# Kernel tuning notes

Hardware: AMD Instinct MI355X
Metric: run time of the kernel (lower is better)

Reference implementation:

```python
import jax, jax.numpy as jnp
import numpy as np

N = 50000
E = 800000
IN_DIM = 64          # 'in_dim'; ndata h has dim 2*in_dim, p has dim in_dim
EDGE_DIM = 32
OUT_DIM = 64
AVG_D_LOG = 2.8332   # avg_d['log'] = log(avg_degree + 1), avg_degree = 16
EPS_STD = 1e-5
EPS_BN = 1e-5


def setup_inputs() -> dict:
    key = jax.random.key(0)
    ks = jax.random.split(key, 16)
    def glorot(k, fan_in, fan_out):
        lim = np.sqrt(6.0 / (fan_in + fan_out)).astype(np.float32)
        return jax.random.uniform(k, (fan_in, fan_out), jnp.float32, -lim, lim)
    d_pre_h = 2 * 2 * IN_DIM + EDGE_DIM   # 288
    d_pre_p = 2 * IN_DIM + EDGE_DIM       # 160
    d_post_h = (4 * 3 + 2) * IN_DIM       # 896
    d_post_p = (4 * 3 + 1) * IN_DIM       # 832
    return {
        "h": jax.random.normal(ks[0], (N, 2 * IN_DIM), jnp.float32),
        "p": jax.random.normal(ks[1], (N, IN_DIM), jnp.float32),
        "e": jax.random.normal(ks[2], (E, EDGE_DIM), jnp.float32),
        "src": jax.random.randint(ks[3], (E,), 0, N, jnp.int32),
        "dst": jax.random.randint(ks[4], (E,), 0, N, jnp.int32),
        "snorm_n": jax.random.uniform(ks[5], (N, 1), jnp.float32, 0.05, 1.0),
        "W_pre_h": glorot(ks[6], d_pre_h, IN_DIM),
        "b_pre_h": jnp.zeros((IN_DIM,), jnp.float32),
        "W_pre_p": glorot(ks[7], d_pre_p, IN_DIM),
        "b_pre_p": jnp.zeros((IN_DIM,), jnp.float32),
        "W_post_h": glorot(ks[8], d_post_h, OUT_DIM),
        "b_post_h": jnp.zeros((OUT_DIM,), jnp.float32),
        "W_post_p": glorot(ks[9], d_post_p, OUT_DIM),
        "b_post_p": jnp.zeros((OUT_DIM,), jnp.float32),
        "bn_gamma": jnp.ones((OUT_DIM,), jnp.float32),
        "bn_beta": jnp.zeros((OUT_DIM,), jnp.float32),
    }


def _agg_scale(msg, dst, deg):
    # msg: [E, d] edge messages reduced at dst; PNA aggregators mean/max/min/std
    degc = jnp.maximum(deg, 1.0)
    s = jax.ops.segment_sum(msg, dst, num_segments=N)
    mean = s / degc[:, None]
    sq = jax.ops.segment_sum(msg * msg, dst, num_segments=N) / degc[:, None]
    var = jax.nn.relu(sq - mean * mean)
    std = jnp.sqrt(var + EPS_STD)
    has = (deg > 0)[:, None]
    mx = jnp.where(has, jax.ops.segment_max(msg, dst, num_segments=N), 0.0)
    mn = jnp.where(has, jax.ops.segment_min(msg, dst, num_segments=N), 0.0)
    agg = jnp.concatenate([mean, mx, mn, std], axis=1)  # [N, 4d]
    logd = jnp.where(deg > 0, jnp.log(deg + 1.0), 1.0)
    amp = (logd / AVG_D_LOG)[:, None]
    att = (AVG_D_LOG / logd)[:, None]
    # scalers: identity, amplification, attenuation -> [N, 12d]
    return jnp.concatenate([agg, agg * amp, agg * att], axis=1)


def reference(h, p, e, src, dst, snorm_n,
              W_pre_h, b_pre_h, W_pre_p, b_pre_p,
              W_post_h, b_post_h, W_post_p, b_post_p,
              bn_gamma, bn_beta):
    # pretrans (1-layer MLP == linear) on concatenated edge endpoint features
    z_h = jnp.concatenate([h[src], h[dst], e], axis=1)   # [E, 4*in+edge]
    z_p = jnp.concatenate([p[src], p[dst], e], axis=1)   # [E, 2*in+edge]
    e_for_h = z_h @ W_pre_h + b_pre_h                    # [E, in]
    e_for_p = z_p @ W_pre_p + b_pre_p                    # [E, in]

    deg = jax.ops.segment_sum(jnp.ones((E,), jnp.float32), dst, num_segments=N)
    agg_h = _agg_scale(e_for_h, dst, deg)                # [N, 12*in]
    agg_p = _agg_scale(e_for_p, dst, deg)                # [N, 12*in]

    h_cat = jnp.concatenate([h, agg_h], axis=1)          # [N, 14*in]
    p_cat = jnp.concatenate([p, agg_p], axis=1)          # [N, 13*in]
    h_out = h_cat @ W_post_h + b_post_h                  # [N, out]
    p_out = p_cat @ W_post_p + b_post_p                  # [N, out]

    # graph norm
    h_out = h_out * snorm_n
    # batch norm (training-mode batch statistics, biased variance)
    mu = jnp.mean(h_out, axis=0)
    var = jnp.mean((h_out - mu) ** 2, axis=0)
    h_out = (h_out - mu) / jnp.sqrt(var + EPS_BN) * bn_gamma + bn_beta
    # dropout = identity (eval / p=0)
    return h_out, p_out
```

## Files before the change

kernel.cpp:

```cpp
#include <hip/hip_runtime.h>
#include <hip/hip_bf16.h>
#include <hip/hip_fp16.h>


#define N_NODES 50000
#define N_EDGES 800000
#define NS 3200000
#define AVG_D_LOG 2.8332f

typedef unsigned short u16;
typedef unsigned int u32;
typedef __attribute__((ext_vector_type(8))) short short8;
typedef __attribute__((ext_vector_type(4))) float f32x4;

__device__ __forceinline__ float bflo(u32 u) { return __uint_as_float(u << 16); }
__device__ __forceinline__ float bfhi(u32 u) { return __uint_as_float(u & 0xffff0000u); }
__device__ __forceinline__ float bf2f(u16 u) { return __uint_as_float(((u32)u) << 16); }
__device__ __forceinline__ u16 f2bf(float x) {
  u32 u = __float_as_uint(x);
  return (u16)((u + 0x7fff + ((u >> 16) & 1)) >> 16);
}
__device__ __forceinline__ float hlo(u32 u) { return __half2float(__ushort_as_half((u16)(u & 0xffffu))); }
__device__ __forceinline__ float hhi(u32 u) { return __half2float(__ushort_as_half((u16)(u >> 16))); }

__device__ __forceinline__ int is_bf(const void* gamma) {
  return ((const u32*)gamma)[0] == 0x3F803F80u ? 1 : 0;
}

__device__ __forceinline__ f32x4 mfma16(short8 a, short8 b, f32x4 c) {
  return __builtin_amdgcn_mfma_f32_16x16x32_bf16(a, b, c, 0, 0, 0);
}

__device__ __forceinline__ void load8(float z[8], const void* base, size_t off,
                                      int bf) {
  if (bf) {
    uint4 u = *(const uint4*)((const u16*)base + off);
    z[0] = bflo(u.x); z[1] = bfhi(u.x); z[2] = bflo(u.y); z[3] = bfhi(u.y);
    z[4] = bflo(u.z); z[5] = bfhi(u.z); z[6] = bflo(u.w); z[7] = bfhi(u.w);
  } else {
    const float* f = (const float*)base + off;
    float4 a = *(const float4*)f;
    float4 b = *(const float4*)(f + 4);
    z[0] = a.x; z[1] = a.y; z[2] = a.z; z[3] = a.w;
    z[4] = b.x; z[5] = b.y; z[6] = b.z; z[7] = b.w;
  }
}

__device__ __forceinline__ float load1(const void* base, size_t off, int bf) {
  return bf ? bf2f(((const u16*)base)[off]) : ((const float*)base)[off];
}

__device__ __forceinline__ short8 cvt8bf(const float z[8]) {
  union { __hip_bfloat162 b[4]; short8 s; } u;
  u.b[0] = __float22bfloat162_rn(make_float2(z[0], z[1]));
  u.b[1] = __float22bfloat162_rn(make_float2(z[2], z[3]));
  u.b[2] = __float22bfloat162_rn(make_float2(z[4], z[5]));
  u.b[3] = __float22bfloat162_rn(make_float2(z[6], z[7]));
  return u.s;
}

__device__ __forceinline__ u32 packh2(float a, float b) {
  union { __half2 h; u32 u; } x;
  x.h = __float22half2_rn(make_float2(a, b));
  return x.u;
}

__device__ __forceinline__ int sem(int o) {
  return ((o >> 4) & 3) * 64 + (o >> 6) * 16 + (o & 15);
}

__global__ __launch_bounds__(256) void k_convert(
    const void* __restrict__ Wpreh, const void* __restrict__ Wprep,
    const void* __restrict__ Wposth, const void* __restrict__ Wpostp,
    const void* __restrict__ bpreh, const void* __restrict__ bprep,
    const void* __restrict__ bposth, const void* __restrict__ bpostp,
    const void* __restrict__ gamma, float* __restrict__ bias,
    u16* __restrict__ frag) {
  int i = blockIdx.x * 256 + threadIdx.x;
  if (i >= 256 + 139264) return;
  int bf = is_bf(gamma);
  if (i < 256) {
    const void* s = (i < 64) ? bpreh : (i < 128) ? bprep : (i < 192) ? bposth : bpostp;
    bias[i] = load1(s, i & 63, bf);
    return;
  }
  int g = i - 256;
  const void* W; int fidx, rowoff, post = 0;
  if (g < 8192)        { W = Wpreh;  fidx = g;          rowoff = 0; }
  else if (g < 16384)  { W = Wpreh;  fidx = g - 8192;   rowoff = 128; }
  else if (g < 20480)  { W = Wprep;  fidx = g - 16384;  rowoff = 0; }
  else if (g < 24576)  { W = Wprep;  fidx = g - 20480;  rowoff = 64; }
  else if (g < 81920)  { W = Wposth; fidx = g - 24576;  rowoff = 0; post = 1; }
  else if (g < 135168) { W = Wpostp; fidx = g - 81920;  rowoff = 0; post = 2; }
  else if (g < 137216) { W = Wpreh;  fidx = g - 135168; rowoff = 256; }
  else                 { W = Wprep;  fidx = g - 137216; rowoff = 128; }
  int f = fidx;
  int kc = f >> 11, nt = (f >> 9) & 3, lane = (f >> 3) & 63, j = f & 7;
  int k = kc * 32 + (lane >> 4) * 8 + j;
  int n = nt * 16 + (lane & 15);
  int row;
  if (post == 1) {
    row = (k < 128) ? k
        : (k < 384) ? 128 + sem(k - 128)
        : (k < 640) ? 384 + sem(k - 384)
                    : 640 + sem(k - 640);
  } else if (post == 2) {
    row = (k < 64) ? k
        : (k < 320) ? 64 + sem(k - 64)
        : (k < 576) ? 320 + sem(k - 320)
                    : 576 + sem(k - 576);
  } else {
    row = rowoff + k;
  }
  frag[g] = f2bf(load1(W, (size_t)row * 64 + n, bf));
}

__global__ __launch_bounds__(256) void k_hist(const int* __restrict__ dst,
                                              int* __restrict__ cnt) {
  int i = blockIdx.x * 256 + threadIdx.x;
  if (i < N_EDGES) atomicAdd(cnt + dst[i], 1);
}

__global__ __launch_bounds__(1024) void k_scan1(const int* __restrict__ cnt,
                                                int* __restrict__ offs,
                                                int* __restrict__ bsum) {
  __shared__ int buf[1024];
  int t = threadIdx.x;
  int i = blockIdx.x * 1024 + t;
  int v = (i < N_NODES) ? cnt[i] : 0;
  buf[t] = v;
  __syncthreads();
#pragma unroll
  for (int d = 1; d < 1024; d <<= 1) {
    int x = (t >= d) ? buf[t - d] : 0;
    __syncthreads();
    buf[t] += x;
    __syncthreads();
  }
  if (i < N_NODES) offs[i] = buf[t] - v;
  if (t == 1023) bsum[blockIdx.x] = buf[1023];
}
__global__ void k_scan2(const int* __restrict__ bsum, int* __restrict__ boff,
                        int* __restrict__ offs, int nb) {
  int t = threadIdx.x;
  int own = (t < nb) ? bsum[t] : 0;
  int v = own;
#pragma unroll
  for (int d = 1; d < 64; d <<= 1) {
    int x = __shfl_up(v, d);
    if (t >= d) v += x;
  }
  if (t < nb) boff[t] = v - own;
  if (t == nb - 1) offs[N_NODES] = v;
}
__global__ __launch_bounds__(256) void k_scan3(int* __restrict__ offs,
                                               const int* __restrict__ boff,
                                               int* __restrict__ cur) {
  int i = blockIdx.x * 256 + threadIdx.x;
  if (i < N_NODES) {
    int v = offs[i] + boff[i >> 10];
    offs[i] = v;
    cur[i] = v;
  }
}

__global__ __launch_bounds__(256) void k_order(const int* __restrict__ src,
                                               const int* __restrict__ dst,
                                               int* __restrict__ cur,
                                               int2* __restrict__ epack) {
  int i = blockIdx.x * 256 + threadIdx.x;
  if (i < N_EDGES) {
    int pos = atomicAdd(cur + dst[i], 1);
    epack[pos] = make_int2(i, src[i]);
  }
}

__global__ __launch_bounds__(256) void k_uproj(
    const void* __restrict__ h, const void* __restrict__ p,
    const float* __restrict__ bias, const u16* __restrict__ frag,
    const void* __restrict__ gamma, u32* __restrict__ Usrc,
    u32* __restrict__ Udst) {
  int wid = (blockIdx.x * 256 + threadIdx.x) >> 6;
  int lane = threadIdx.x & 63;
  if (wid >= 6250) return;
  int part = wid / 3125;
  int node0 = (wid % 3125) * 16;
  int bf = is_bf(gamma);
  const u16* bfrH = frag + (part ? 8192 : 0);
  const u16* bfrP = frag + (part ? 20480 : 16384);
  u32* U = part ? Udst : Usrc;
  int m = lane & 15, quad = lane >> 4;
  f32x4 accH[4], accP[4];
#pragma unroll
  for (int nt = 0; nt < 4; ++nt) {
    accH[nt] = (f32x4){0.f, 0.f, 0.f, 0.f};
    accP[nt] = (f32x4){0.f, 0.f, 0.f, 0.f};
  }
#pragma unroll
  for (int kc = 0; kc < 4; ++kc) {
    float z[8];
    load8(z, h, (size_t)(node0 + m) * 128 + kc * 32 + quad * 8, bf);
    short8 a = cvt8bf(z);
#pragma unroll
    for (int nt = 0; nt < 4; ++nt) {
      short8 b = *(const short8*)(bfrH + (size_t)((kc * 4 + nt) * 64 + lane) * 8);
      accH[nt] = mfma16(a, b, accH[nt]);
    }
  }
#pragma unroll
  for (int kc = 0; kc < 2; ++kc) {
    float z[8];
    load8(z, p, (size_t)(node0 + m) * 64 + kc * 32 + quad * 8, bf);
    short8 a = cvt8bf(z);
#pragma unroll
    for (int nt = 0; nt < 4; ++nt) {
      short8 b = *(const short8*)(bfrP + (size_t)((kc * 4 + nt) * 64 + lane) * 8);
      accP[nt] = mfma16(a, b, accP[nt]);
    }
  }
#pragma unroll
  for (int r = 0; r < 4; ++r) {
    int node = node0 + quad * 4 + r;
#pragma unroll
    for (int nt = 0; nt < 4; ++nt) {
      int col = nt * 16 + m;
      float vh = accH[nt][r] + (part ? bias[col] : 0.f);
      float vp = accP[nt][r] + (part ? bias[64 + col] : 0.f);
      U[(size_t)node * 64 + col] = packh2(vh, vp);
    }
  }
}

template <int BF>
__global__ __launch_bounds__(256, 4) void k_aggf(
    const void* __restrict__ e, const int2* __restrict__ epack,
    const int* __restrict__ offs, const u32* __restrict__ Us32,
    const u32* __restrict__ Ud32, const u16* __restrict__ Wfh,
    const u16* __restrict__ Wfp, const void* __restrict__ gamma,
    u16* __restrict__ Ah, u16* __restrict__ Ap, float* __restrict__ degf) {
  if (is_bf(gamma) != BF) return;
  int n = blockIdx.x * 4 + (threadIdx.x >> 6);
  int lane = threadIdx.x & 63;
  if (n >= N_NODES) return;
  int m = lane & 15, quad = lane >> 4;
  int s = offs[n], epos = offs[n + 1];
  int deg = epos - s;

  short8 bh[4], bp[4];
#pragma unroll
  for (int nt = 0; nt < 4; ++nt) {
    bh[nt] = *(const short8*)(Wfh + (size_t)(nt * 64 + lane) * 8);
    bp[nt] = *(const short8*)(Wfp + (size_t)(nt * 64 + lane) * 8);
  }
  float uhd[4], upd[4];
#pragma unroll
  for (int nt = 0; nt < 4; ++nt) {
    u32 u = Ud32[(size_t)n * 64 + nt * 16 + m];
    uhd[nt] = hlo(u); upd[nt] = hhi(u);
  }
  float hsum[4], hsq[4], hmx[4], hmn[4], psum[4], psq[4], pmx[4], pmn[4];
#pragma unroll
  for (int nt = 0; nt < 4; ++nt) {
    hsum[nt] = hsq[nt] = psum[nt] = psq[nt] = 0.f;
    hmx[nt] = pmx[nt] = -3.4e38f;
    hmn[nt] = pmn[nt] = 3.4e38f;
  }

  int full = deg & ~15;
  int c0 = 0;
  for (; c0 < full; c0 += 16) {
    int eid = epack[s + c0 + m].x;
    int b0 = s + c0 + quad * 4;
    int sce0 = epack[b0].y, sce1 = epack[b0 + 1].y;
    int sce2 = epack[b0 + 2].y, sce3 = epack[b0 + 3].y;
    u32 usv0[4], usv1[4], usv2[4], usv3[4];
#pragma unroll
    for (int nt = 0; nt < 4; ++nt) {
      usv0[nt] = Us32[(size_t)sce0 * 64 + nt * 16 + m];
      usv1[nt] = Us32[(size_t)sce1 * 64 + nt * 16 + m];
      usv2[nt] = Us32[(size_t)sce2 * 64 + nt * 16 + m];
      usv3[nt] = Us32[(size_t)sce3 * 64 + nt * 16 + m];
    }
    short8 a;
    if (BF) {
      a = *(const short8*)((const u16*)e + (size_t)eid * 32 + quad * 8);
    } else {
      float z[8];
      load8(z, e, (size_t)eid * 32 + quad * 8, 0);
      a = cvt8bf(z);
    }
    {
      f32x4 acc[4];
#pragma unroll
      for (int nt = 0; nt < 4; ++nt)
        acc[nt] = mfma16(a, bh[nt], (f32x4){0.f, 0.f, 0.f, 0.f});
#pragma unroll
      for (int nt = 0; nt < 4; ++nt) {
        float w0 = acc[nt][0] + hlo(usv0[nt]);
        float w1 = acc[nt][1] + hlo(usv1[nt]);
        float w2 = acc[nt][2] + hlo(usv2[nt]);
        float w3 = acc[nt][3] + hlo(usv3[nt]);
        hmx[nt] = fmaxf(fmaxf(hmx[nt], w0), fmaxf(fmaxf(w1, w2), w3));
        hmn[nt] = fminf(fminf(hmn[nt], w0), fminf(fminf(w1, w2), w3));
        hsum[nt] += (w0 + w1) + (w2 + w3);
        hsq[nt] = fmaf(w0, w0, fmaf(w1, w1, fmaf(w2, w2, fmaf(w3, w3, hsq[nt]))));
      }
    }
    {
      f32x4 acc[4];
#pragma unroll
      for (int nt = 0; nt < 4; ++nt)
        acc[nt] = mfma16(a, bp[nt], (f32x4){0.f, 0.f, 0.f, 0.f});
#pragma unroll
      for (int nt = 0; nt < 4; ++nt) {
        float w0 = acc[nt][0] + hhi(usv0[nt]);
        float w1 = acc[nt][1] + hhi(usv1[nt]);
        float w2 = acc[nt][2] + hhi(usv2[nt]);
        float w3 = acc[nt][3] + hhi(usv3[nt]);
        pmx[nt] = fmaxf(fmaxf(pmx[nt], w0), fmaxf(fmaxf(w1, w2), w3));
        pmn[nt] = fminf(fminf(pmn[nt], w0), fminf(fminf(w1, w2), w3));
        psum[nt] += (w0 + w1) + (w2 + w3);
        psq[nt] = fmaf(w0, w0, fmaf(w1, w1, fmaf(w2, w2, fmaf(w3, w3, psq[nt]))));
      }
    }
  }
  if (c0 < deg) {
    int im = s + c0 + m; im = im < epos ? im : epos - 1;
    int eid = epack[im].x;
    int b0 = s + c0 + quad * 4;
    int i0 = b0 < epos ? b0 : epos - 1;
    int i1 = b0 + 1 < epos ? b0 + 1 : epos - 1;
    int i2 = b0 + 2 < epos ? b0 + 2 : epos - 1;
    int i3 = b0 + 3 < epos ? b0 + 3 : epos - 1;
    int sce0 = epack[i0].y, sce1 = epack[i1].y;
    int sce2 = epack[i2].y, sce3 = epack[i3].y;
    u32 usv0[4], usv1[4], usv2[4], usv3[4];
#pragma unroll
    for (int nt = 0; nt < 4; ++nt) {
      usv0[nt] = Us32[(size_t)sce0 * 64 + nt * 16 + m];
      usv1[nt] = Us32[(size_t)sce1 * 64 + nt * 16 + m];
      usv2[nt] = Us32[(size_t)sce2 * 64 + nt * 16 + m];
      usv3[nt] = Us32[(size_t)sce3 * 64 + nt * 16 + m];
    }
    short8 a;
    if (BF) {
      a = *(const short8*)((const u16*)e + (size_t)eid * 32 + quad * 8);
    } else {
      float z[8];
      load8(z, e, (size_t)eid * 32 + quad * 8, 0);
      a = cvt8bf(z);
    }
    bool v0 = (c0 + quad * 4 + 0) < deg;
    bool v1 = (c0 + quad * 4 + 1) < deg;
    bool v2 = (c0 + quad * 4 + 2) < deg;
    bool v3 = (c0 + quad * 4 + 3) < deg;
    {
      f32x4 acc[4];
#pragma unroll
      for (int nt = 0; nt < 4; ++nt)
        acc[nt] = mfma16(a, bh[nt], (f32x4){0.f, 0.f, 0.f, 0.f});
#pragma unroll
      for (int nt = 0; nt < 4; ++nt) {
        float w0 = acc[nt][0] + hlo(usv0[nt]);
        float w1 = acc[nt][1] + hlo(usv1[nt]);
        float w2 = acc[nt][2] + hlo(usv2[nt]);
        float w3 = acc[nt][3] + hlo(usv3[nt]);
        hmx[nt] = fmaxf(fmaxf(hmx[nt], w0), fmaxf(fmaxf(w1, w2), w3));
        hmn[nt] = fminf(fminf(hmn[nt], w0), fminf(fminf(w1, w2), w3));
        float z0 = v0 ? w0 : 0.f, z1 = v1 ? w1 : 0.f;
        float z2 = v2 ? w2 : 0.f, z3 = v3 ? w3 : 0.f;
        hsum[nt] += (z0 + z1) + (z2 + z3);
        hsq[nt] = fmaf(z0, z0, fmaf(z1, z1, fmaf(z2, z2, fmaf(z3, z3, hsq[nt]))));
      }
    }
    {
      f32x4 acc[4];
#pragma unroll
      for (int nt = 0; nt < 4; ++nt)
        acc[nt] = mfma16(a, bp[nt], (f32x4){0.f, 0.f, 0.f, 0.f});
#pragma unroll
      for (int nt = 0; nt < 4; ++nt) {
        float w0 = acc[nt][0] + hhi(usv0[nt]);
        float w1 = acc[nt][1] + hhi(usv1[nt]);
        float w2 = acc[nt][2] + hhi(usv2[nt]);
        float w3 = acc[nt][3] + hhi(usv3[nt]);
        pmx[nt] = fmaxf(fmaxf(pmx[nt], w0), fmaxf(fmaxf(w1, w2), w3));
        pmn[nt] = fminf(fminf(pmn[nt], w0), fminf(fminf(w1, w2), w3));
        float z0 = v0 ? w0 : 0.f, z1 = v1 ? w1 : 0.f;
        float z2 = v2 ? w2 : 0.f, z3 = v3 ? w3 : 0.f;
        psum[nt] += (z0 + z1) + (z2 + z3);
        psq[nt] = fmaf(z0, z0, fmaf(z1, z1, fmaf(z2, z2, fmaf(z3, z3, psq[nt]))));
      }
    }
  }

  float dv = (float)deg;
  bool has = deg > 0;
  float inv = has ? 1.f / dv : 1.f;
  if (lane == 0) degf[n] = dv;

#pragma unroll
  for (int nt = 0; nt < 4; ++nt) {
    hsum[nt] += __shfl_xor(hsum[nt], 16); hsum[nt] += __shfl_xor(hsum[nt], 32);
    hsq[nt] += __shfl_xor(hsq[nt], 16);   hsq[nt] += __shfl_xor(hsq[nt], 32);
    hmx[nt] = fmaxf(hmx[nt], __shfl_xor(hmx[nt], 16));
    hmx[nt] = fmaxf(hmx[nt], __shfl_xor(hmx[nt], 32));
    hmn[nt] = fminf(hmn[nt], __shfl_xor(hmn[nt], 16));
    hmn[nt] = fminf(hmn[nt], __shfl_xor(hmn[nt], 32));
    psum[nt] += __shfl_xor(psum[nt], 16); psum[nt] += __shfl_xor(psum[nt], 32);
    psq[nt] += __shfl_xor(psq[nt], 16);   psq[nt] += __shfl_xor(psq[nt], 32);
    pmx[nt] = fmaxf(pmx[nt], __shfl_xor(pmx[nt], 16));
    pmx[nt] = fmaxf(pmx[nt], __shfl_xor(pmx[nt], 32));
    pmn[nt] = fminf(pmn[nt], __shfl_xor(pmn[nt], 16));
    pmn[nt] = fminf(pmn[nt], __shfl_xor(pmn[nt], 32));
  }

#pragma unroll
  for (int nt = 0; nt < 4; ++nt) {
    {
      float mean_w = hsum[nt] * inv;
      float var = fmaf(-mean_w, mean_w, hsq[nt] * inv);
      var = var > 0.f ? var : 0.f;
      float sd = sqrtf(var + 1e-5f);
      float o = quad == 0 ? (has ? mean_w + uhd[nt] : 0.f)
              : quad == 1 ? (has ? hmx[nt] + uhd[nt] : 0.f)
              : quad == 2 ? (has ? hmn[nt] + uhd[nt] : 0.f) : sd;
      Ah[(size_t)n * 256 + nt * 64 + lane] = f2bf(o);
    }
    {
      float mean_w = psum[nt] * inv;
      float var = fmaf(-mean_w, mean_w, psq[nt] * inv);
      var = var > 0.f ? var : 0.f;
      float sd = sqrtf(var + 1e-5f);
      float o = quad == 0 ? (has ? mean_w + upd[nt] : 0.f)
              : quad == 1 ? (has ? pmx[nt] + upd[nt] : 0.f)
              : quad == 2 ? (has ? pmn[nt] + upd[nt] : 0.f) : sd;
      Ap[(size_t)n * 256 + nt * 64 + lane] = f2bf(o);
    }
  }
}

__global__ __launch_bounds__(256) void k_node(
    const void* __restrict__ h, const void* __restrict__ p,
    const u16* __restrict__ Ah, const u16* __restrict__ Ap,
    const void* __restrict__ snorm, const float* __restrict__ degf,
    const u16* __restrict__ BfH, const u16* __restrict__ BfP,
    const float* __restrict__ biasH, const float* __restrict__ biasP,
    const void* __restrict__ gamma, float* __restrict__ outh,
    float* __restrict__ outp) {
  int w = (blockIdx.x * 256 + threadIdx.x) >> 6;
  int lane = threadIdx.x & 63;
  if (w >= N_NODES / 16) return;
  int bf = is_bf(gamma);
  int m = lane & 15, quad = lane >> 4;
  int node0 = w * 16;

  float ampr[4], attr[4];
#pragma unroll
  for (int r = 0; r < 4; ++r) {
    float dv = degf[node0 + quad * 4 + r];
    float logd = (dv > 0.5f) ? logf(dv + 1.f) : 1.f;
    ampr[r] = logd * (1.f / AVG_D_LOG);
    attr[r] = AVG_D_LOG / logd;
  }

  f32x4 accB[4], accA[4], accT[4];
#pragma unroll
  for (int nt = 0; nt < 4; ++nt) {
    accB[nt] = (f32x4){0.f, 0.f, 0.f, 0.f};
    accA[nt] = (f32x4){0.f, 0.f, 0.f, 0.f};
    accT[nt] = (f32x4){0.f, 0.f, 0.f, 0.f};
  }
#pragma unroll 2
  for (int kc = 0; kc < 12; ++kc) {
    short8 a;
    if (kc < 4) {
      float z[8];
      load8(z, h, (size_t)(node0 + m) * 128 + kc * 32 + quad * 8, bf);
      a = cvt8bf(z);
    } else {
      a = *(const short8*)(Ah + (size_t)(node0 + m) * 256 + (kc - 4) * 32 + quad * 8);
    }
#pragma unroll
    for (int nt = 0; nt < 4; ++nt)
      accB[nt] = mfma16(a, *(const short8*)(BfH + (size_t)((kc * 4 + nt) * 64 + lane) * 8), accB[nt]);
    if (kc >= 4) {
      int kk = kc - 4;
#pragma unroll
      for (int nt = 0; nt < 4; ++nt)
        accA[nt] = mfma16(a, *(const short8*)(BfH + 24576 + (size_t)((kk * 4 + nt) * 64 + lane) * 8), accA[nt]);
#pragma unroll
      for (int nt = 0; nt < 4; ++nt)
        accT[nt] = mfma16(a, *(const short8*)(BfH + 40960 + (size_t)((kk * 4 + nt) * 64 + lane) * 8), accT[nt]);
    }
  }
  float bH[4];
#pragma unroll
  for (int nt = 0; nt < 4; ++nt) bH[nt] = biasH[nt * 16 + m];
#pragma unroll
  for (int r = 0; r < 4; ++r) {
    int node = node0 + quad * 4 + r;
    float sn = load1(snorm, node, bf);
#pragma unroll
    for (int nt = 0; nt < 4; ++nt) {
      float v = accB[nt][r] + ampr[r] * accA[nt][r] + attr[r] * accT[nt][r] + bH[nt];
      outh[(size_t)node * 64 + nt * 16 + m] = v * sn;
    }
  }

#pragma unroll
  for (int nt = 0; nt < 4; ++nt) {
    accB[nt] = (f32x4){0.f, 0.f, 0.f, 0.f};
    accA[nt] = (f32x4){0.f, 0.f, 0.f, 0.f};
    accT[nt] = (f32x4){0.f, 0.f, 0.f, 0.f};
  }
#pragma unroll 2
  for (int kc = 0; kc < 10; ++kc) {
    short8 a;
    if (kc < 2) {
      float z[8];
      load8(z, p, (size_t)(node0 + m) * 64 + kc * 32 + quad * 8, bf);
      a = cvt8bf(z);
    } else {
      a = *(const short8*)(Ap + (size_t)(node0 + m) * 256 + (kc - 2) * 32 + quad * 8);
    }
#pragma unroll
    for (int nt = 0; nt < 4; ++nt)
      accB[nt] = mfma16(a, *(const short8*)(BfP + (size_t)((kc * 4 + nt) * 64 + lane) * 8), accB[nt]);
    if (kc >= 2) {
      int kk = kc - 2;
#pragma unroll
      for (int nt = 0; nt < 4; ++nt)
        accA[nt] = mfma16(a, *(const short8*)(BfP + 20480 + (size_t)((kk * 4 + nt) * 64 + lane) * 8), accA[nt]);
#pragma unroll
      for (int nt = 0; nt < 4; ++nt)
        accT[nt] = mfma16(a, *(const short8*)(BfP + 36864 + (size_t)((kk * 4 + nt) * 64 + lane) * 8), accT[nt]);
    }
  }
  float bP[4];
#pragma unroll
  for (int nt = 0; nt < 4; ++nt) bP[nt] = biasP[nt * 16 + m];
#pragma unroll
  for (int r = 0; r < 4; ++r) {
    int node = node0 + quad * 4 + r;
#pragma unroll
    for (int nt = 0; nt < 4; ++nt) {
      float v = accB[nt][r] + ampr[r] * accA[nt][r] + attr[r] * accT[nt][r] + bP[nt];
      outp[(size_t)node * 64 + nt * 16 + m] = v;
    }
  }
}

__global__ __launch_bounds__(256) void k_bnstats(const float* __restrict__ hpre,
                                                 float* __restrict__ bnacc) {
  int j = threadIdx.x & 63;
  float s = 0.0f, q = 0.0f;
  for (int n = blockIdx.x * 4 + (threadIdx.x >> 6); n < N_NODES;
       n += gridDim.x * 4) {
    float x = hpre[(size_t)n * 64 + j];
    s += x; q += x * x;
  }
  __shared__ float ls[256], lq[256];
  ls[threadIdx.x] = s; lq[threadIdx.x] = q;
  __syncthreads();
  if (threadIdx.x < 64) {
    s = ls[threadIdx.x] + ls[threadIdx.x + 64] + ls[threadIdx.x + 128] + ls[threadIdx.x + 192];
    q = lq[threadIdx.x] + lq[threadIdx.x + 64] + lq[threadIdx.x + 128] + lq[threadIdx.x + 192];
    atomicAdd(bnacc + threadIdx.x, s);
    atomicAdd(bnacc + 64 + threadIdx.x, q);
  }
}

__global__ __launch_bounds__(256) void k_bnapply(
    float* __restrict__ outh, const float* __restrict__ bnacc,
    const void* __restrict__ gamma, const void* __restrict__ beta) {
  int i = blockIdx.x * 256 + threadIdx.x;
  if (i >= NS) return;
  int bf = is_bf(gamma);
  int j = i & 63;
  const float invN = 1.0f / (float)N_NODES;
  float mu = bnacc[j] * invN;
  float var = fmaf(-mu, mu, bnacc[64 + j] * invN);
  var = var > 0.0f ? var : 0.0f;
  float sc = load1(gamma, j, bf) * rsqrtf(var + 1e-5f);
  float sh = load1(beta, j, bf) - mu * sc;
  outh[i] = fmaf(outh[i], sc, sh);
}

extern "C" void kernel_launch(void* const* d_in, const int* in_sizes, int n_in,
                              void* d_out, int out_size, void* d_ws,
                              size_t ws_size, hipStream_t stream) {
  const void* h = d_in[0];
  const void* p = d_in[1];
  const void* e = d_in[2];
  const int* src = (const int*)d_in[3];
  const int* dst = (const int*)d_in[4];
  const void* snorm = d_in[5];
  const void* Wpreh = d_in[6];
  const void* bpreh = d_in[7];
  const void* Wprep = d_in[8];
  const void* bprep = d_in[9];
  const void* Wposth = d_in[10];
  const void* bposth = d_in[11];
  const void* Wpostp = d_in[12];
  const void* bpostp = d_in[13];
  const void* gamma = d_in[14];
  const void* beta = d_in[15];

  float* ws = (float*)d_ws;
  u32* Usrc = (u32*)ws;
  u32* Udst = (u32*)(ws + 3200000L);
  u16* Ah = (u16*)(ws + 6400000L);
  u16* Ap = (u16*)(ws + 12800000L);
  int2* epack = (int2*)(ws + 19200000L);
  int* cnt = (int*)(ws + 20800016L);
  int* offs = (int*)(ws + 20850016L);
  float* degf = ws + 20900020L;
  int* cur = (int*)(ws + 20950020L);
  int* bsum = (int*)(ws + 21000020L);
  int* boff = (int*)(ws + 21000084L);
  float* bnacc = ws + 21000148L;
  float* bias = ws + 21000276L;
  u16* frag = (u16*)(ws + 21000532L);

  u16* fragPostH = frag + 24576;
  u16* fragPostP = frag + 81920;
  u16* fragWehF = frag + 135168;
  u16* fragWepF = frag + 137216;

  float* outh = (float*)d_out;
  float* outp = outh + (size_t)NS;

  int bfh = -1;
  if (in_sizes && n_in >= 16) {
    if (in_sizes[0] == 25600000) bfh = 0;
    else if (in_sizes[0] == 12800000) bfh = 1;
  }

  hipMemsetAsync(cnt, 0, N_NODES * sizeof(int), stream);
  hipMemsetAsync(bnacc, 0, 128 * sizeof(float), stream);
  k_convert<<<(256 + 139264 + 255) / 256, 256, 0, stream>>>(
      Wpreh, Wprep, Wposth, Wpostp, bpreh, bprep, bposth, bpostp, gamma, bias,
      frag);
  k_hist<<<(N_EDGES + 255) / 256, 256, 0, stream>>>(dst, cnt);
  const int NB = (N_NODES + 1023) / 1024;
  k_scan1<<<NB, 1024, 0, stream>>>(cnt, offs, bsum);
  k_scan2<<<1, 64, 0, stream>>>(bsum, boff, offs, NB);
  k_scan3<<<(N_NODES + 255) / 256, 256, 0, stream>>>(offs, boff, cur);
  k_order<<<(N_EDGES + 255) / 256, 256, 0, stream>>>(src, dst, cur, epack);
  k_uproj<<<(6250 + 3) / 4, 256, 0, stream>>>(h, p, bias, frag, gamma, Usrc,
                                              Udst);
  if (bfh != 1)
    k_aggf<0><<<(N_NODES + 3) / 4, 256, 0, stream>>>(
        e, epack, offs, Usrc, Udst, fragWehF, fragWepF, gamma, Ah, Ap, degf);
  if (bfh != 0)
    k_aggf<1><<<(N_NODES + 3) / 4, 256, 0, stream>>>(
        e, epack, offs, Usrc, Udst, fragWehF, fragWepF, gamma, Ah, Ap, degf);
  k_node<<<(N_NODES / 16 + 3) / 4, 256, 0, stream>>>(
      h, p, Ah, Ap, snorm, degf, fragPostH, fragPostP, bias + 128, bias + 192,
      gamma, outh, outp);
  k_bnstats<<<256, 256, 0, stream>>>(outh, bnacc);
  k_bnapply<<<(NS + 255) / 256, 256, 0, stream>>>(outh, bnacc, gamma, beta);
}
```

Baseline: 503.2 us.

## Fuse memsets, scan stages and BN stats; split node towers across warps

```diff
diff --git a/kernel.cpp b/kernel.cpp
--- a/kernel.cpp
+++ b/kernel.cpp
@@ -75,9 +75,14 @@
     const void* __restrict__ bpreh, const void* __restrict__ bprep,
     const void* __restrict__ bposth, const void* __restrict__ bpostp,
     const void* __restrict__ gamma, float* __restrict__ bias,
-    u16* __restrict__ frag) {
+    u16* __restrict__ frag, int* __restrict__ cnt, float* __restrict__ bnacc) {
   int i = blockIdx.x * 256 + threadIdx.x;
-  if (i >= 256 + 139264) return;
+  if (i >= 256 + 139264) {
+    int z = i - (256 + 139264);
+    if (z < N_NODES) cnt[z] = 0;
+    else if (z < N_NODES + 128) bnacc[z - N_NODES] = 0.0f;
+    return;
+  }
   int bf = is_bf(gamma);
   if (i < 256) {
     const void* s = (i < 64) ? bpreh : (i < 128) ? bprep : (i < 192) ? bposth : bpostp;
@@ -140,28 +145,29 @@
   if (i < N_NODES) offs[i] = buf[t] - v;
   if (t == 1023) bsum[blockIdx.x] = buf[1023];
 }
-__global__ void k_scan2(const int* __restrict__ bsum, int* __restrict__ boff,
-                        int* __restrict__ offs, int nb) {
+
+__global__ __launch_bounds__(256) void k_scan23(int* __restrict__ offs,
+                                                const int* __restrict__ bsum,
+                                                int* __restrict__ cur) {
+  const int nb = (N_NODES + 1023) >> 10;
   int t = threadIdx.x;
-  int own = (t < nb) ? bsum[t] : 0;
-  int v = own;
+  int lane = t & 63;
+  int i = blockIdx.x * 256 + t;
+  int myb = blockIdx.x >> 2;
+  int v = (lane < nb) ? bsum[lane] : 0;
+  int pre = (lane < myb) ? v : 0;
+  int tot = v;
 #pragma unroll
   for (int d = 1; d < 64; d <<= 1) {
-    int x = __shfl_up(v, d);
-    if (t >= d) v += x;
-  }
-  if (t < nb) boff[t] = v - own;
-  if (t == nb - 1) offs[N_NODES] = v;
-}
-__global__ __launch_bounds__(256) void k_scan3(int* __restrict__ offs,
-                                               const int* __restrict__ boff,
-                                               int* __restrict__ cur) {
-  int i = blockIdx.x * 256 + threadIdx.x;
+    pre += __shfl_xor(pre, d);
+    tot += __shfl_xor(tot, d);
+  }
   if (i < N_NODES) {
-    int v = offs[i] + boff[i >> 10];
-    offs[i] = v;
-    cur[i] = v;
-  }
+    int o = offs[i] + pre;
+    offs[i] = o;
+    cur[i] = o;
+  }
+  if (blockIdx.x == 0 && t == 0) offs[N_NODES] = tot;
 }
 
 __global__ __launch_bounds__(256) void k_order(const int* __restrict__ src,
@@ -232,7 +238,7 @@
 }
 
 template <int BF>
-__global__ __launch_bounds__(256, 4) void k_aggf(
+__global__ __launch_bounds__(256, 8) void k_aggf(
     const void* __restrict__ e, const int2* __restrict__ epack,
     const int* __restrict__ offs, const u32* __restrict__ Us32,
     const u32* __restrict__ Ud32, const u16* __restrict__ Wfh,
@@ -447,127 +453,130 @@
     const u16* __restrict__ BfH, const u16* __restrict__ BfP,
     const float* __restrict__ biasH, const float* __restrict__ biasP,
     const void* __restrict__ gamma, float* __restrict__ outh,
-    float* __restrict__ outp) {
-  int w = (blockIdx.x * 256 + threadIdx.x) >> 6;
+    float* __restrict__ outp, float* __restrict__ bnacc) {
+  const int NW = N_NODES / 16;
+  int gw = (blockIdx.x * 256 + threadIdx.x) >> 6;
   int lane = threadIdx.x & 63;
-  if (w >= N_NODES / 16) return;
   int bf = is_bf(gamma);
   int m = lane & 15, quad = lane >> 4;
-  int node0 = w * 16;
-
-  float ampr[4], attr[4];
-#pragma unroll
-  for (int r = 0; r < 4; ++r) {
-    float dv = degf[node0 + quad * 4 + r];
-    float logd = (dv > 0.5f) ? logf(dv + 1.f) : 1.f;
-    ampr[r] = logd * (1.f / AVG_D_LOG);
-    attr[r] = AVG_D_LOG / logd;
-  }
-
-  f32x4 accB[4], accA[4], accT[4];
-#pragma unroll
-  for (int nt = 0; nt < 4; ++nt) {
-    accB[nt] = (f32x4){0.f, 0.f, 0.f, 0.f};
-    accA[nt] = (f32x4){0.f, 0.f, 0.f, 0.f};
-    accT[nt] = (f32x4){0.f, 0.f, 0.f, 0.f};
-  }
+
+  __shared__ float bsumS[64], bsqS[64];
+  if (threadIdx.x < 64) { bsumS[threadIdx.x] = 0.f; bsqS[threadIdx.x] = 0.f; }
+  __syncthreads();
+
+  int tower = (gw >= NW) ? 1 : 0;
+  int w = tower ? gw - NW : gw;
+  bool active = gw < 2 * NW;
+  float hs[4] = {0.f, 0.f, 0.f, 0.f}, hq[4] = {0.f, 0.f, 0.f, 0.f};
+
+  if (active) {
+    int node0 = w * 16;
+    float ampr[4], attr[4];
+#pragma unroll
+    for (int r = 0; r < 4; ++r) {
+      float dv = degf[node0 + quad * 4 + r];
+      float logd = (dv > 0.5f) ? logf(dv + 1.f) : 1.f;
+      ampr[r] = logd * (1.f / AVG_D_LOG);
+      attr[r] = AVG_D_LOG / logd;
+    }
+    f32x4 accB[4], accA[4], accT[4];
+#pragma unroll
+    for (int nt = 0; nt < 4; ++nt) {
+      accB[nt] = (f32x4){0.f, 0.f, 0.f, 0.f};
+      accA[nt] = (f32x4){0.f, 0.f, 0.f, 0.f};
+      accT[nt] = (f32x4){0.f, 0.f, 0.f, 0.f};
+    }
+    if (tower == 0) {
 #pragma unroll 2
-  for (int kc = 0; kc < 12; ++kc) {
-    short8 a;
-    if (kc < 4) {
-      float z[8];
-      load8(z, h, (size_t)(node0 + m) * 128 + kc * 32 + quad * 8, bf);
-      a = cvt8bf(z);
+      for (int kc = 0; kc < 12; ++kc) {
+        short8 a;
+        if (kc < 4) {
+          float z[8];
+          load8(z, h, (size_t)(node0 + m) * 128 + kc * 32 + quad * 8, bf);
+          a = cvt8bf(z);
+        } else {
+          a = *(const short8*)(Ah + (size_t)(node0 + m) * 256 + (kc - 4) * 32 + quad * 8);
+        }
+#pragma unroll
+        for (int nt = 0; nt < 4; ++nt)
+          accB[nt] = mfma16(a, *(const short8*)(BfH + (size_t)((kc * 4 + nt) * 64 + lane) * 8), accB[nt]);
+        if (kc >= 4) {
+          int kk = kc - 4;
+#pragma unroll
+          for (int nt = 0; nt < 4; ++nt)
+            accA[nt] = mfma16(a, *(const short8*)(BfH + 24576 + (size_t)((kk * 4 + nt) * 64 + lane) * 8), accA[nt]);
+#pragma unroll
+          for (int nt = 0; nt < 4; ++nt)
+            accT[nt] = mfma16(a, *(const short8*)(BfH + 40960 + (size_t)((kk * 4 + nt) * 64 + lane) * 8), accT[nt]);
+        }
+      }
+      float bH[4];
+#pragma unroll
+      for (int nt = 0; nt < 4; ++nt) bH[nt] = biasH[nt * 16 + m];
+#pragma unroll
+      for (int r = 0; r < 4; ++r) {
+        int node = node0 + quad * 4 + r;
+        float sn = load1(snorm, node, bf);
+#pragma unroll
+        for (int nt = 0; nt < 4; ++nt) {
+          float v = (accB[nt][r] + ampr[r] * accA[nt][r] + attr[r] * accT[nt][r] + bH[nt]) * sn;
+          outh[(size_t)node * 64 + nt * 16 + m] = v;
+          hs[nt] += v;
+          hq[nt] = fmaf(v, v, hq[nt]);
+        }
+      }
     } else {
-      a = *(const short8*)(Ah + (size_t)(node0 + m) * 256 + (kc - 4) * 32 + quad * 8);
-    }
-#pragma unroll
-    for (int nt = 0; nt < 4; ++nt)
-      accB[nt] = mfma16(a, *(const short8*)(BfH + (size_t)((kc * 4 + nt) * 64 + lane) * 8), accB[nt]);
-    if (kc >= 4) {
-      int kk = kc - 4;
-#pragma unroll
-      for (int nt = 0; nt < 4; ++nt)
-        accA[nt] = mfma16(a, *(const short8*)(BfH + 24576 + (size_t)((kk * 4 + nt) * 64 + lane) * 8), accA[nt]);
-#pragma unroll
-      for (int nt = 0; nt < 4; ++nt)
-        accT[nt] = mfma16(a, *(const short8*)(BfH + 40960 + (size_t)((kk * 4 + nt) * 64 + lane) * 8), accT[nt]);
-    }
-  }
-  float bH[4];
-#pragma unroll
-  for (int nt = 0; nt < 4; ++nt) bH[nt] = biasH[nt * 16 + m];
-#pragma unroll
-  for (int r = 0; r < 4; ++r) {
-    int node = node0 + quad * 4 + r;
-    float sn = load1(snorm, node, bf);
+#pragma unroll 2
+      for (int kc = 0; kc < 10; ++kc) {
+        short8 a;
+        if (kc < 2) {
+          float z[8];
+          load8(z, p, (size_t)(node0 + m) * 64 + kc * 32 + quad * 8, bf);
+          a = cvt8bf(z);
+        } else {
+          a = *(const short8*)(Ap + (size_t)(node0 + m) * 256 + (kc - 2) * 32 + quad * 8);
+        }
+#pragma unroll
+        for (int nt = 0; nt < 4; ++nt)
+          accB[nt] = mfma16(a, *(const short8*)(BfP + (size_t)((kc * 4 + nt) * 64 + lane) * 8), accB[nt]);
+        if (kc >= 2) {
+          int kk = kc - 2;
+#pragma unroll
+          for (int nt = 0; nt < 4; ++nt)
+            accA[nt] = mfma16(a, *(const short8*)(BfP + 20480 + (size_t)((kk * 4 + nt) * 64 + lane) * 8), accA[nt]);
+#pragma unroll
+          for (int nt = 0; nt < 4; ++nt)
+            accT[nt] = mfma16(a, *(const short8*)(BfP + 36864 + (size_t)((kk * 4 + nt) * 64 + lane) * 8), accT[nt]);
+        }
+      }
+      float bP[4];
+#pragma unroll
+      for (int nt = 0; nt < 4; ++nt) bP[nt] = biasP[nt * 16 + m];
+#pragma unroll
+      for (int r = 0; r < 4; ++r) {
+        int node = node0 + quad * 4 + r;
+#pragma unroll
+        for (int nt = 0; nt < 4; ++nt) {
+          float v = accB[nt][r] + ampr[r] * accA[nt][r] + attr[r] * accT[nt][r] + bP[nt];
+          outp[(size_t)node * 64 + nt * 16 + m] = v;
+        }
+      }
+    }
+  }
+
+  if (active && tower == 0) {
 #pragma unroll
     for (int nt = 0; nt < 4; ++nt) {
-      float v = accB[nt][r] + ampr[r] * accA[nt][r] + attr[r] * accT[nt][r] + bH[nt];
-      outh[(size_t)node * 64 + nt * 16 + m] = v * sn;
-    }
-  }
-
-#pragma unroll
-  for (int nt = 0; nt < 4; ++nt) {
-    accB[nt] = (f32x4){0.f, 0.f, 0.f, 0.f};
-    accA[nt] = (f32x4){0.f, 0.f, 0.f, 0.f};
-    accT[nt] = (f32x4){0.f, 0.f, 0.f, 0.f};
-  }
-#pragma unroll 2
-  for (int kc = 0; kc < 10; ++kc) {
-    short8 a;
-    if (kc < 2) {
-      float z[8];
-      load8(z, p, (size_t)(node0 + m) * 64 + kc * 32 + quad * 8, bf);
-      a = cvt8bf(z);
-    } else {
-      a = *(const short8*)(Ap + (size_t)(node0 + m) * 256 + (kc - 2) * 32 + quad * 8);
-    }
-#pragma unroll
-    for (int nt = 0; nt < 4; ++nt)
-      accB[nt] = mfma16(a, *(const short8*)(BfP + (size_t)((kc * 4 + nt) * 64 + lane) * 8), accB[nt]);
-    if (kc >= 2) {
-      int kk = kc - 2;
-#pragma unroll
-      for (int nt = 0; nt < 4; ++nt)
-        accA[nt] = mfma16(a, *(const short8*)(BfP + 20480 + (size_t)((kk * 4 + nt) * 64 + lane) * 8), accA[nt]);
-#pragma unroll
-      for (int nt = 0; nt < 4; ++nt)
-        accT[nt] = mfma16(a, *(const short8*)(BfP + 36864 + (size_t)((kk * 4 + nt) * 64 + lane) * 8), accT[nt]);
-    }
-  }
-  float bP[4];
-#pragma unroll
-  for (int nt = 0; nt < 4; ++nt) bP[nt] = biasP[nt * 16 + m];
-#pragma unroll
-  for (int r = 0; r < 4; ++r) {
-    int node = node0 + quad * 4 + r;
-#pragma unroll
-    for (int nt = 0; nt < 4; ++nt) {
-      float v = accB[nt][r] + ampr[r] * accA[nt][r] + attr[r] * accT[nt][r] + bP[nt];
-      outp[(size_t)node * 64 + nt * 16 + m] = v;
-    }
-  }
-}
-
-__global__ __launch_bounds__(256) void k_bnstats(const float* __restrict__ hpre,
-                                                 float* __restrict__ bnacc) {
-  int j = threadIdx.x & 63;
-  float s = 0.0f, q = 0.0f;
-  for (int n = blockIdx.x * 4 + (threadIdx.x >> 6); n < N_NODES;
-       n += gridDim.x * 4) {
-    float x = hpre[(size_t)n * 64 + j];
-    s += x; q += x * x;
-  }
-  __shared__ float ls[256], lq[256];
-  ls[threadIdx.x] = s; lq[threadIdx.x] = q;
+      atomicAdd(&bsumS[nt * 16 + m], hs[nt]);
+      atomicAdd(&bsqS[nt * 16 + m], hq[nt]);
+    }
+  }
   __syncthreads();
-  if (threadIdx.x < 64) {
-    s = ls[threadIdx.x] + ls[threadIdx.x + 64] + ls[threadIdx.x + 128] + ls[threadIdx.x + 192];
-    q = lq[threadIdx.x] + lq[threadIdx.x + 64] + lq[threadIdx.x + 128] + lq[threadIdx.x + 192];
-    atomicAdd(bnacc + threadIdx.x, s);
-    atomicAdd(bnacc + 64 + threadIdx.x, q);
+  if (blockIdx.x <= (NW - 1) / 4) {
+    if (threadIdx.x < 64)
+      atomicAdd(bnacc + threadIdx.x, bsumS[threadIdx.x]);
+    else if (threadIdx.x < 128)
+      atomicAdd(bnacc + threadIdx.x, bsqS[threadIdx.x - 64]);
   }
 }
 
@@ -618,7 +627,6 @@
   float* degf = ws + 20900020L;
   int* cur = (int*)(ws + 20950020L);
   int* bsum = (int*)(ws + 21000020L);
-  int* boff = (int*)(ws + 21000084L);
   float* bnacc = ws + 21000148L;
   float* bias = ws + 21000276L;
   u16* frag = (u16*)(ws + 21000532L);
@@ -637,16 +645,13 @@
     else if (in_sizes[0] == 12800000) bfh = 1;
   }
 
-  hipMemsetAsync(cnt, 0, N_NODES * sizeof(int), stream);
-  hipMemsetAsync(bnacc, 0, 128 * sizeof(float), stream);
-  k_convert<<<(256 + 139264 + 255) / 256, 256, 0, stream>>>(
+  k_convert<<<(256 + 139264 + N_NODES + 128 + 255) / 256, 256, 0, stream>>>(
       Wpreh, Wprep, Wposth, Wpostp, bpreh, bprep, bposth, bpostp, gamma, bias,
-      frag);
+      frag, cnt, bnacc);
   k_hist<<<(N_EDGES + 255) / 256, 256, 0, stream>>>(dst, cnt);
   const int NB = (N_NODES + 1023) / 1024;
   k_scan1<<<NB, 1024, 0, stream>>>(cnt, offs, bsum);
-  k_scan2<<<1, 64, 0, stream>>>(bsum, boff, offs, NB);
-  k_scan3<<<(N_NODES + 255) / 256, 256, 0, stream>>>(offs, boff, cur);
+  k_scan23<<<(N_NODES + 255) / 256, 256, 0, stream>>>(offs, bsum, cur);
   k_order<<<(N_EDGES + 255) / 256, 256, 0, stream>>>(src, dst, cur, epack);
   k_uproj<<<(6250 + 3) / 4, 256, 0, stream>>>(h, p, bias, frag, gamma, Usrc,
                                               Udst);
@@ -656,9 +661,8 @@
   if (bfh != 0)
     k_aggf<1><<<(N_NODES + 3) / 4, 256, 0, stream>>>(
         e, epack, offs, Usrc, Udst, fragWehF, fragWepF, gamma, Ah, Ap, degf);
-  k_node<<<(N_NODES / 16 + 3) / 4, 256, 0, stream>>>(
+  k_node<<<(2 * (N_NODES / 16) + 3) / 4, 256, 0, stream>>>(
       h, p, Ah, Ap, snorm, degf, fragPostH, fragPostP, bias + 128, bias + 192,
-      gamma, outh, outp);
-  k_bnstats<<<256, 256, 0, stream>>>(outh, bnacc);
+      gamma, outh, outp, bnacc);
   k_bnapply<<<(NS + 255) / 256, 256, 0, stream>>>(outh, bnacc, gamma, beta);
 }
```

Measured after the change: 912.3 us. +81.3%, slower.
